# Optimization experiments

Hardware: AMD Instinct MI355X
Metric: run time of the kernel (lower is better)

Reference implementation:

```python
import jax, jax.numpy as jnp
import numpy as np

B, T, IN, H, NC, NE = 4096, 26, 512, 512, 97, 256

def setup_inputs() -> dict:
    key = jax.random.key(0)
    ks = jax.random.split(key, 9)
    s = 0.02
    return {
        "batch_H": jax.random.normal(ks[0], (B, T, IN), jnp.float32),
        "text": jax.random.randint(ks[1], (B, T), 0, NC + 1, jnp.int32),
        "emb_table": jax.random.normal(ks[2], (NC + 1, NE), jnp.float32) * s,
        "W_ih": jax.random.normal(ks[3], (4 * H, IN + NE), jnp.float32) * s,
        "W_hh": jax.random.normal(ks[4], (4 * H, H), jnp.float32) * s,
        "b_ih": jax.random.normal(ks[5], (4 * H,), jnp.float32) * s,
        "b_hh": jax.random.normal(ks[6], (4 * H,), jnp.float32) * s,
        "W_gen": jax.random.normal(ks[7], (NC, H), jnp.float32) * s,
        "b_gen": jax.random.normal(ks[8], (NC,), jnp.float32) * s,
    }

def reference(batch_H, text, emb_table, W_ih, W_hh, b_ih, b_hh, W_gen, b_gen):
    # char embeddings for every step: [B, T, NE]
    emb = emb_table[text]
    # LSTM input per step: concat(encoder feature, char embedding) -> [B, T, IN+NE]
    x = jnp.concatenate([batch_H, emb], axis=-1)
    # precompute input-to-hidden gate contributions for all steps: [T, B, 4H]
    gx = jnp.einsum('bti,gi->tbg', x, W_ih) + b_ih

    h0 = jnp.zeros((batch_H.shape[0], W_hh.shape[1]), batch_H.dtype)
    c0 = jnp.zeros_like(h0)

    def step(carry, gx_t):
        h, c = carry
        gates = gx_t + h @ W_hh.T + b_hh  # [B, 4H]
        i, f, g, o = jnp.split(gates, 4, axis=-1)  # PyTorch LSTMCell gate order
        i = jax.nn.sigmoid(i); f = jax.nn.sigmoid(f)
        g = jnp.tanh(g); o = jax.nn.sigmoid(o)
        c_new = f * c + i * g
        h_new = o * jnp.tanh(c_new)
        return (h_new, c_new), h_new

    _, hs = jax.lax.scan(step, (h0, c0), gx)  # hs: [T, B, H]
    output_hiddens = jnp.transpose(hs, (1, 0, 2))  # [B, T, H]
    probs = jnp.einsum('bth,ch->btc', output_hiddens, W_gen) + b_gen
    return probs, output_hiddens
```

## Files before the change

kernel.cpp:

```cpp
#include <hip/hip_runtime.h>
#include <stdint.h>

#define B_   4096
#define T_   26
#define NC_  97
#define PROBS_SZ ((size_t)B_*T_*NC_)

using frag8 = __attribute__((ext_vector_type(8))) short;
using f32x4 = __attribute__((ext_vector_type(4))) float;

__device__ inline unsigned short f2bf(float f) {
  unsigned u = __float_as_uint(f);
  return (unsigned short)((u + 0x7fffu + ((u >> 16) & 1u)) >> 16);
}
__device__ inline float bf2f(unsigned short h) {
  return __uint_as_float(((unsigned)h) << 16);
}
__device__ inline float sigf(float x) { return 1.f / (1.f + __expf(-x)); }
__device__ inline float tanh_(float x) {
  float e = __expf(2.f * x);
  return 1.f - 2.f / (e + 1.f);
}

__device__ inline void gld16(const void* g, void* l) {
  __builtin_amdgcn_global_load_lds(
      (const __attribute__((address_space(1))) void*)g,
      (__attribute__((address_space(3))) void*)l, 16, 0, 0);
}

__device__ inline int perm_to_orig(int p) {
  int tile = p >> 7, wn = (p >> 6) & 1, gate = (p >> 4) & 3, ul = p & 15;
  return gate * 512 + tile * 32 + wn * 16 + ul;
}

__device__ inline void chunk(const unsigned short* __restrict__ Ab, size_t lda,
                             const unsigned short* __restrict__ Bb, size_t ldb,
                             unsigned short* As, unsigned short* Bs, f32x4 acc[4][4]) {
  const int tid = threadIdx.x;
  const int r4 = tid >> 2, c8 = (tid & 3) * 8;
  const int lane = tid & 63, w = tid >> 6;
  const int wm = w >> 1, wn = w & 1, l15 = lane & 15, quad = lane >> 4;
  gld16(Ab + (size_t)r4 * lda + c8,        (char*)As + tid * 16);
  gld16(Ab + (size_t)(r4 + 64) * lda + c8, (char*)As + 4096 + tid * 16);
  gld16(Bb + (size_t)r4 * ldb + c8,        (char*)Bs + tid * 16);
  gld16(Bb + (size_t)(r4 + 64) * ldb + c8, (char*)Bs + 4096 + tid * 16);
  __syncthreads();
  frag8 a[4], b[4];
#pragma unroll
  for (int i = 0; i < 4; i++)
    a[i] = *(const frag8*)(As + (wm * 64 + i * 16 + l15) * 32 + quad * 8);
#pragma unroll
  for (int i = 0; i < 4; i++)
    b[i] = *(const frag8*)(Bs + (wn * 64 + i * 16 + l15) * 32 + quad * 8);
#pragma unroll
  for (int i = 0; i < 4; i++)
#pragma unroll
    for (int j = 0; j < 4; j++)
      acc[i][j] = __builtin_amdgcn_mfma_f32_16x16x32_bf16(a[i], b[j], acc[i][j], 0, 0, 0);
  __syncthreads();
}

__global__ void k_cast_x(const float* __restrict__ x, unsigned short* __restrict__ o) {
  long i = (long)blockIdx.x * 256 + threadIdx.x;
  const float4* p = (const float4*)x;
  float4 a = p[i * 2], b = p[i * 2 + 1];
  frag8 r;
  r[0] = (short)f2bf(a.x); r[1] = (short)f2bf(a.y);
  r[2] = (short)f2bf(a.z); r[3] = (short)f2bf(a.w);
  r[4] = (short)f2bf(b.x); r[5] = (short)f2bf(b.y);
  r[6] = (short)f2bf(b.z); r[7] = (short)f2bf(b.w);
  *(frag8*)(o + i * 8) = r;
}

__global__ void k_prep_w(const float* __restrict__ Wih, const float* __restrict__ Whh,
                         const float* __restrict__ Wgen,
                         unsigned short* __restrict__ wcomb,
                         unsigned short* __restrict__ wgenp) {
  int gid = blockIdx.x * 256 + threadIdx.x;
  if (gid < 2097152) {
    int p = gid >> 10, k = gid & 1023;
    int g = perm_to_orig(p);
    float v = (k < 512) ? Wih[(size_t)g * 768 + k] : Whh[(size_t)g * 512 + (k - 512)];
    wcomb[gid] = f2bf(v);
  } else {
    int lid = gid - 2097152;
    int n = lid >> 9, k = lid & 511;
    wgenp[lid] = (n < NC_) ? f2bf(Wgen[(size_t)n * 512 + k]) : 0;
  }
}

__global__ void k_wembT(const float* __restrict__ Wih, float* __restrict__ wt) {
  int gid = blockIdx.x * 256 + threadIdx.x;
  int e = gid >> 11, p = gid & 2047;
  wt[gid] = Wih[(size_t)perm_to_orig(p) * 768 + 512 + e];
}

__global__ void k_tc(const float* __restrict__ emb, const float* __restrict__ wt,
                     const float* __restrict__ bih, const float* __restrict__ bhh,
                     float* __restrict__ tc) {
  int gid = blockIdx.x * 256 + threadIdx.x;
  int cls = gid >> 11, p = gid & 2047;
  int g = perm_to_orig(p);
  float s = bih[g] + bhh[g];
  const float* er = emb + (size_t)cls * 256;
#pragma unroll 4
  for (int e = 0; e < 256; e++) s += er[e] * wt[(size_t)e * 2048 + p];
  tc[gid] = s;
}

__global__ __launch_bounds__(256, 2) void k_step(const unsigned short* __restrict__ X,
                                                 const unsigned short* __restrict__ hs,
                                                 const unsigned short* __restrict__ W,
                                                 const float* __restrict__ tc,
                                                 const int* __restrict__ text,
                                                 float* __restrict__ cbuf,
                                                 unsigned short* hsw,
                                                 float* __restrict__ outH, int t) {
  __shared__ unsigned short As[128 * 32], Bs[128 * 32];
  f32x4 acc[4][4];
#pragma unroll
  for (int i = 0; i < 4; i++)
#pragma unroll
    for (int j = 0; j < 4; j++) acc[i][j] = (f32x4){0.f, 0.f, 0.f, 0.f};
  const int n0 = blockIdx.x * 128, m0 = blockIdx.y * 128;
  const unsigned short* A0 = X + (size_t)t * 512 + (size_t)m0 * 13312;
  const unsigned short* A1 = hs + (size_t)(t > 0 ? t - 1 : 0) * 512 + (size_t)m0 * 13312;
  const unsigned short* Bb = W + (size_t)n0 * 1024;
  const int Keff = t ? 1024 : 512;
  for (int k0 = 0; k0 < Keff; k0 += 32) {
    const unsigned short* Ab = (k0 < 512) ? A0 + k0 : A1 + (k0 - 512);
    chunk(Ab, 13312, Bb + k0, 1024, As, Bs, acc);
  }
  const int tid = threadIdx.x, lane = tid & 63, w = tid >> 6;
  const int wm = w >> 1, wn = w & 1, l15 = lane & 15, quad = lane >> 4;
  const int j = (n0 >> 2) + wn * 16 + l15;
  const int colb = n0 + wn * 64 + l15;
#pragma unroll
  for (int fr = 0; fr < 4; fr++) {
#pragma unroll
    for (int reg = 0; reg < 4; reg++) {
      int r = m0 + wm * 64 + fr * 16 + quad * 4 + reg;
      int cls = text[r * 26 + t];
      const float* tcr = tc + (size_t)cls * 2048 + colb;
      float p0 = acc[fr][0][reg] + tcr[0];
      float p1 = acc[fr][1][reg] + tcr[16];
      float p2 = acc[fr][2][reg] + tcr[32];
      float p3 = acc[fr][3][reg] + tcr[48];
      float cp = t ? cbuf[(size_t)r * 512 + j] : 0.f;
      float ii = sigf(p0), ff = sigf(p1), gg = tanh_(p2), oo = sigf(p3);
      float cn = ff * cp + ii * gg;
      float h = oo * tanh_(cn);
      cbuf[(size_t)r * 512 + j] = cn;
      hsw[((size_t)r * 26 + t) * 512 + j] = f2bf(h);
      outH[((size_t)r * 26 + t) * 512 + j] = h;
    }
  }
}

__global__ __launch_bounds__(256, 2) void k_probs(const unsigned short* __restrict__ hs,
                                                  const unsigned short* __restrict__ Wg,
                                                  const float* __restrict__ bg,
                                                  float* __restrict__ out) {
  __shared__ unsigned short As[128 * 32], Bs[128 * 32];
  f32x4 acc[4][4];
#pragma unroll
  for (int i = 0; i < 4; i++)
#pragma unroll
    for (int j = 0; j < 4; j++) acc[i][j] = (f32x4){0.f, 0.f, 0.f, 0.f};
  const int m0 = blockIdx.x * 128;
  for (int k0 = 0; k0 < 512; k0 += 32)
    chunk(hs + (size_t)m0 * 512 + k0, 512, Wg + k0, 512, As, Bs, acc);
  const int tid = threadIdx.x, lane = tid & 63, w = tid >> 6;
  const int wm = w >> 1, wn = w & 1, l15 = lane & 15, quad = lane >> 4;
#pragma unroll
  for (int fr = 0; fr < 4; fr++) {
#pragma unroll
    for (int reg = 0; reg < 4; reg++) {
      int m = m0 + wm * 64 + fr * 16 + quad * 4 + reg;
#pragma unroll
      for (int fc = 0; fc < 4; fc++) {
        int col = wn * 64 + fc * 16 + l15;
        if (col < NC_) out[(size_t)m * NC_ + col] = acc[fr][fc][reg] + bg[col];
      }
    }
  }
}

extern "C" void kernel_launch(void* const* d_in, const int* in_sizes, int n_in,
                              void* d_out, int out_size, void* d_ws, size_t ws_size,
                              hipStream_t stream) {
  const float* batch_H = (const float*)d_in[0];
  const int*   text    = (const int*)d_in[1];
  const float* emb     = (const float*)d_in[2];
  const float* W_ih    = (const float*)d_in[3];
  const float* W_hh    = (const float*)d_in[4];
  const float* b_ih    = (const float*)d_in[5];
  const float* b_hh    = (const float*)d_in[6];
  const float* W_gen   = (const float*)d_in[7];
  const float* b_gen   = (const float*)d_in[8];
  float* out = (float*)d_out;
  char* ws = (char*)d_ws;

  unsigned short* X     = (unsigned short*)(ws + 0);
  unsigned short* hs    = (unsigned short*)(ws + 109051904ULL);
  float*          cbuf  = (float*)(ws + 218103808ULL);
  unsigned short* wcomb = (unsigned short*)(ws + 226492416ULL);
  unsigned short* wgenp = (unsigned short*)(ws + 230686720ULL);
  float*          tc    = (float*)(ws + 230817792ULL);
  float*          wembT = (float*)(ws + 231620608ULL);

  k_cast_x<<<26624, 256, 0, stream>>>(batch_H, X);
  k_prep_w<<<8448, 256, 0, stream>>>(W_ih, W_hh, W_gen, wcomb, wgenp);
  k_wembT<<<2048, 256, 0, stream>>>(W_ih, wembT);
  k_tc<<<784, 256, 0, stream>>>(emb, wembT, b_ih, b_hh, tc);
  for (int t = 0; t < 26; t++)
    k_step<<<dim3(16, 32), 256, 0, stream>>>(X, hs, wcomb, tc, text, cbuf, hs,
                                             out + PROBS_SZ, t);
  k_probs<<<832, 256, 0, stream>>>(hs, wgenp, b_gen, out);
}
```

Baseline: 1.399 ms.

## Fuse LSTM timesteps into one persistent kernel with per-group atomic barriers

```diff
diff --git a/kernel.cpp b/kernel.cpp
--- a/kernel.cpp
+++ b/kernel.cpp
@@ -12,9 +12,6 @@
 __device__ inline unsigned short f2bf(float f) {
   unsigned u = __float_as_uint(f);
   return (unsigned short)((u + 0x7fffu + ((u >> 16) & 1u)) >> 16);
-}
-__device__ inline float bf2f(unsigned short h) {
-  return __uint_as_float(((unsigned)h) << 16);
 }
 __device__ inline float sigf(float x) { return 1.f / (1.f + __expf(-x)); }
 __device__ inline float tanh_(float x) {
@@ -108,52 +105,73 @@
   tc[gid] = s;
 }
 
-__global__ __launch_bounds__(256, 2) void k_step(const unsigned short* __restrict__ X,
-                                                 const unsigned short* __restrict__ hs,
+__global__ void k_zero(int* p) { p[threadIdx.x] = 0; }
+
+__global__ __launch_bounds__(256, 2) void k_lstm(const unsigned short* __restrict__ X,
+                                                 unsigned short* __restrict__ hs,
                                                  const unsigned short* __restrict__ W,
                                                  const float* __restrict__ tc,
                                                  const int* __restrict__ text,
-                                                 float* __restrict__ cbuf,
-                                                 unsigned short* hsw,
-                                                 float* __restrict__ outH, int t) {
+                                                 float* __restrict__ outH,
+                                                 int* __restrict__ ctr) {
   __shared__ unsigned short As[128 * 32], Bs[128 * 32];
-  f32x4 acc[4][4];
-#pragma unroll
-  for (int i = 0; i < 4; i++)
-#pragma unroll
-    for (int j = 0; j < 4; j++) acc[i][j] = (f32x4){0.f, 0.f, 0.f, 0.f};
-  const int n0 = blockIdx.x * 128, m0 = blockIdx.y * 128;
-  const unsigned short* A0 = X + (size_t)t * 512 + (size_t)m0 * 13312;
-  const unsigned short* A1 = hs + (size_t)(t > 0 ? t - 1 : 0) * 512 + (size_t)m0 * 13312;
-  const unsigned short* Bb = W + (size_t)n0 * 1024;
-  const int Keff = t ? 1024 : 512;
-  for (int k0 = 0; k0 < Keff; k0 += 32) {
-    const unsigned short* Ab = (k0 < 512) ? A0 + k0 : A1 + (k0 - 512);
-    chunk(Ab, 13312, Bb + k0, 1024, As, Bs, acc);
-  }
+  const int gid = blockIdx.x;
+  const int g = gid >> 4;
+  const int n0 = (gid & 15) * 128;
+  const int m0 = g * 128;
   const int tid = threadIdx.x, lane = tid & 63, w = tid >> 6;
   const int wm = w >> 1, wn = w & 1, l15 = lane & 15, quad = lane >> 4;
   const int j = (n0 >> 2) + wn * 16 + l15;
   const int colb = n0 + wn * 64 + l15;
-#pragma unroll
-  for (int fr = 0; fr < 4; fr++) {
-#pragma unroll
-    for (int reg = 0; reg < 4; reg++) {
-      int r = m0 + wm * 64 + fr * 16 + quad * 4 + reg;
-      int cls = text[r * 26 + t];
-      const float* tcr = tc + (size_t)cls * 2048 + colb;
-      float p0 = acc[fr][0][reg] + tcr[0];
-      float p1 = acc[fr][1][reg] + tcr[16];
-      float p2 = acc[fr][2][reg] + tcr[32];
-      float p3 = acc[fr][3][reg] + tcr[48];
-      float cp = t ? cbuf[(size_t)r * 512 + j] : 0.f;
-      float ii = sigf(p0), ff = sigf(p1), gg = tanh_(p2), oo = sigf(p3);
-      float cn = ff * cp + ii * gg;
-      float h = oo * tanh_(cn);
-      cbuf[(size_t)r * 512 + j] = cn;
-      hsw[((size_t)r * 26 + t) * 512 + j] = f2bf(h);
-      outH[((size_t)r * 26 + t) * 512 + j] = h;
+  const unsigned short* Bb = W + (size_t)n0 * 1024;
+  float creg[16];
+#pragma unroll
+  for (int i = 0; i < 16; i++) creg[i] = 0.f;
+
+  for (int t = 0; t < 26; t++) {
+    f32x4 acc[4][4];
+#pragma unroll
+    for (int i = 0; i < 4; i++)
+#pragma unroll
+      for (int jj = 0; jj < 4; jj++) acc[i][jj] = (f32x4){0.f, 0.f, 0.f, 0.f};
+    const unsigned short* A0 = X + (size_t)t * 512 + (size_t)m0 * 13312;
+    for (int k0 = 0; k0 < 512; k0 += 32)
+      chunk(A0 + k0, 13312, Bb + k0, 1024, As, Bs, acc);
+    if (t > 0) {
+      if (tid == 0) {
+        while (__hip_atomic_load(&ctr[g], __ATOMIC_ACQUIRE,
+                                 __HIP_MEMORY_SCOPE_AGENT) < 16 * t)
+          __builtin_amdgcn_s_sleep(8);
+      }
+      __syncthreads();
+      __threadfence();
+      const unsigned short* A1 = hs + (size_t)(t - 1) * (B_ * 512) + (size_t)m0 * 512;
+      for (int k0 = 0; k0 < 512; k0 += 32)
+        chunk(A1 + k0, 512, Bb + 512 + k0, 1024, As, Bs, acc);
     }
+#pragma unroll
+    for (int fr = 0; fr < 4; fr++) {
+#pragma unroll
+      for (int reg = 0; reg < 4; reg++) {
+        int r = m0 + wm * 64 + fr * 16 + quad * 4 + reg;
+        int cls = text[r * 26 + t];
+        const float* tcr = tc + (size_t)cls * 2048 + colb;
+        float p0 = acc[fr][0][reg] + tcr[0];
+        float p1 = acc[fr][1][reg] + tcr[16];
+        float p2 = acc[fr][2][reg] + tcr[32];
+        float p3 = acc[fr][3][reg] + tcr[48];
+        float ii = sigf(p0), ff = sigf(p1), gg = tanh_(p2), oo = sigf(p3);
+        float cn = ff * creg[fr * 4 + reg] + ii * gg;
+        float h = oo * tanh_(cn);
+        creg[fr * 4 + reg] = cn;
+        hs[(size_t)t * (B_ * 512) + (size_t)r * 512 + j] = f2bf(h);
+        outH[((size_t)r * 26 + t) * 512 + j] = h;
+      }
+    }
+    __threadfence();
+    __syncthreads();
+    if (tid == 0)
+      __hip_atomic_fetch_add(&ctr[g], 1, __ATOMIC_RELEASE, __HIP_MEMORY_SCOPE_AGENT);
   }
 }
 
@@ -176,11 +194,13 @@
   for (int fr = 0; fr < 4; fr++) {
 #pragma unroll
     for (int reg = 0; reg < 4; reg++) {
-      int m = m0 + wm * 64 + fr * 16 + quad * 4 + reg;
+      int mp = m0 + wm * 64 + fr * 16 + quad * 4 + reg;
+      int t = mp >> 12, r = mp & 4095;
+      size_t ob = ((size_t)r * 26 + t) * NC_;
 #pragma unroll
       for (int fc = 0; fc < 4; fc++) {
         int col = wn * 64 + fc * 16 + l15;
-        if (col < NC_) out[(size_t)m * NC_ + col] = acc[fr][fc][reg] + bg[col];
+        if (col < NC_) out[ob + col] = acc[fr][fc][reg] + bg[col];
       }
     }
   }
@@ -203,18 +223,17 @@
 
   unsigned short* X     = (unsigned short*)(ws + 0);
   unsigned short* hs    = (unsigned short*)(ws + 109051904ULL);
-  float*          cbuf  = (float*)(ws + 218103808ULL);
-  unsigned short* wcomb = (unsigned short*)(ws + 226492416ULL);
-  unsigned short* wgenp = (unsigned short*)(ws + 230686720ULL);
-  float*          tc    = (float*)(ws + 230817792ULL);
-  float*          wembT = (float*)(ws + 231620608ULL);
-
+  unsigned short* wcomb = (unsigned short*)(ws + 218103808ULL);
+  unsigned short* wgenp = (unsigned short*)(ws + 222298112ULL);
+  float*          tc    = (float*)(ws + 222429184ULL);
+  float*          wembT = (float*)(ws + 223232000ULL);
+  int*            ctr   = (int*)(ws + 225329152ULL);
+
+  k_zero<<<1, 32, 0, stream>>>(ctr);
   k_cast_x<<<26624, 256, 0, stream>>>(batch_H, X);
   k_prep_w<<<8448, 256, 0, stream>>>(W_ih, W_hh, W_gen, wcomb, wgenp);
   k_wembT<<<2048, 256, 0, stream>>>(W_ih, wembT);
   k_tc<<<784, 256, 0, stream>>>(emb, wembT, b_ih, b_hh, tc);
-  for (int t = 0; t < 26; t++)
-    k_step<<<dim3(16, 32), 256, 0, stream>>>(X, hs, wcomb, tc, text, cbuf, hs,
-                                             out + PROBS_SZ, t);
+  k_lstm<<<512, 256, 0, stream>>>(X, hs, wcomb, tc, text, out + PROBS_SZ, ctr);
   k_probs<<<832, 256, 0, stream>>>(hs, wgenp, b_gen, out);
 }
```

Measured after the change: 4.778 ms. 242% more time.
